# Optimization experiments

Hardware: AMD Instinct MI355X
Metric: run time of the kernel (lower is better)

## Reference

```python
import jax, jax.numpy as jnp
import numpy as np

# IR-Net EDE surrogate-gradient constants (ir_1w1a.IRConv2d defaults)
K = 10.0
T = 0.1
BN_EPS = 1e-5

@jax.custom_vjp
def binary_quantize(x):
    return jnp.sign(x)

def _bq_fwd(x):
    return jnp.sign(x), x

def _bq_bwd(x, g):
    # grad = k * t * (1 - tanh(x*t)^2) * g   (IR-Net BinaryQuantize.backward)
    return (K * T * (1.0 - jnp.tanh(x * T) ** 2) * g,)

binary_quantize.defvjp(_bq_fwd, _bq_bwd)


def setup_inputs() -> dict:
    key = jax.random.key(0)
    k1, k2 = jax.random.split(key, 2)
    return {
        "x": jax.random.normal(k1, (32, 256, 56, 56), dtype=jnp.float32),
        "weight": jax.random.normal(k2, (256, 256, 3, 3), dtype=jnp.float32) * 0.05,
        "gamma": jnp.ones((256,), dtype=jnp.float32),
        "beta": jnp.zeros((256,), dtype=jnp.float32),
    }


def _convalg(x, weight, gamma, beta):
    co = weight.shape[0]
    wf = weight.reshape(co, -1)
    # per-output-channel standardization of weights
    bw = weight - wf.mean(-1).reshape(co, 1, 1, 1)
    std = jnp.std(bw.reshape(co, -1), axis=-1, ddof=1).reshape(co, 1, 1, 1)  # torch unbiased std
    bw = bw / std
    # detached power-of-2 per-channel scale: sw = 2^round(log2(mean|bw|))
    sw = jax.lax.stop_gradient(
        2.0 ** jnp.round(jnp.log2(jnp.abs(bw).reshape(co, -1).mean(-1)))
    ).reshape(co, 1, 1, 1)
    bwq = binary_quantize(bw) * sw   # binarized, scaled weights {-sw, +sw}
    ba = binary_quantize(x)          # binarized activations {-1, +1}
    y = jax.lax.conv_general_dilated(
        ba, bwq,
        window_strides=(1, 1),
        padding=((1, 1), (1, 1)),
        dimension_numbers=("NCHW", "OIHW", "NCHW"),
    )
    # BatchNorm2d, training-mode forward (batch statistics, biased variance)
    mean = y.mean(axis=(0, 2, 3), keepdims=True)
    var = y.var(axis=(0, 2, 3), keepdims=True)
    yn = (y - mean) * jax.lax.rsqrt(var + BN_EPS)
    yn = yn * gamma.reshape(1, -1, 1, 1) + beta.reshape(1, -1, 1, 1)
    # Hardtanh
    return jnp.clip(yn, -1.0, 1.0)


def reference(x, weight, gamma, beta):
    return _convalg(x, weight, gamma, beta)
```

## Files before the change

### kernel.cpp

```cpp
#include <hip/hip_runtime.h>
#include <math.h>

#define HH 56
#define WW 56
#define NB 32
#define CC 256
#define PIX 3136
#define M_TOT 100352
#define PADH 58
#define PADW 58
#define ACTQ_BYTES ((size_t)NB*PADH*PADW*CC)
#define WQ_BYTES ((size_t)9*CC*CC)
#define SBUF_BYTES ((size_t)M_TOT*CC*2)
#define BM 128
#define BN 256

typedef unsigned int u32;
typedef unsigned long long u64;
typedef int v4i __attribute__((ext_vector_type(4)));

typedef const __attribute__((address_space(1))) unsigned int* as1_u32p;
typedef __attribute__((address_space(3))) unsigned int* as3_u32p;
#define GLOAD_LDS16(g, l) \
  __builtin_amdgcn_global_load_lds((as1_u32p)(g), (as3_u32p)(l), 16, 0, 0)

__global__ __launch_bounds__(256) void pack_weights_i8(
    const float* __restrict__ wt, signed char* __restrict__ wq,
    float* __restrict__ swv,
    long long* __restrict__ sumS, long long* __restrict__ sumSS) {
  int co = blockIdx.x;
  int t  = threadIdx.x;
  int lane = t & 63, wid = t >> 6;

  float wv[9];
  const float* wp = wt + ((size_t)co*CC + t)*9;
  double psum = 0.0;
#pragma unroll
  for (int k = 0; k < 9; ++k) { wv[k] = wp[k]; psum += (double)wv[k]; }

  __shared__ double redm[4];
#pragma unroll
  for (int off = 32; off > 0; off >>= 1) psum += __shfl_xor(psum, off);
  if (lane == 0) redm[wid] = psum;
  __syncthreads();
  double mean = (redm[0]+redm[1]+redm[2]+redm[3]) * (1.0/2304.0);

  double pabs = 0.0, psq = 0.0;
#pragma unroll
  for (int k = 0; k < 9; ++k) {
    double d = (double)wv[k] - mean;
    pabs += fabs(d);
    psq  += d*d;
  }
#pragma unroll
  for (int off = 32; off > 0; off >>= 1) {
    pabs += __shfl_xor(pabs, off);
    psq  += __shfl_xor(psq,  off);
  }
  __shared__ double reda[4], redq[4];
  if (lane == 0) { reda[wid] = pabs; redq[wid] = psq; }
  __syncthreads();
  if (t == 0) {
    double sa = reda[0]+reda[1]+reda[2]+reda[3];
    double sq = redq[0]+redq[1]+redq[2]+redq[3];
    double stdv = sqrt(sq / 2303.0);
    double mabs = (sa * (1.0/2304.0)) / stdv;
    swv[co] = (float)exp2(rint(log2(mabs)));
    sumS[co]  = 0;
    sumSS[co] = 0;
  }
#pragma unroll
  for (int k = 0; k < 9; ++k)
    wq[((size_t)k*CC + co)*CC + t] =
        (((double)wv[k] - mean) > 0.0) ? (signed char)1 : (signed char)-1;
}

__global__ __launch_bounds__(256) void pack_acts_i8(
    const float* __restrict__ x, signed char* __restrict__ actq) {
  int n = blockIdx.y, tile = blockIdx.x;
  int lane = threadIdx.x & 63, cw = threadIdx.x >> 6;
  int pp = tile*64 + lane;
  if (pp >= PADH*PADW) return;
  int ph = pp / PADW, pw = pp - ph*PADW;
  signed char* dst = actq + ((size_t)(n*PADH + ph)*PADW + pw)*CC + cw*64;
  if (ph == 0 || ph == PADH-1 || pw == 0 || pw == PADW-1) {
    uint4 z = make_uint4(0u, 0u, 0u, 0u);
#pragma unroll
    for (int q = 0; q < 4; ++q) ((uint4*)dst)[q] = z;
    return;
  }
  int h = ph - 1, w = pw - 1;
  const float* xp = x + ((size_t)(n*CC + cw*64))*PIX + h*WW + w;
  u32 wrd[16];
#pragma unroll
  for (int c16 = 0; c16 < 16; ++c16) {
    u32 v = 0;
#pragma unroll
    for (int b = 0; b < 4; ++b) {
      float f = xp[(size_t)(c16*4 + b)*PIX];
      v |= (f > 0.0f ? 0x01u : 0xFFu) << (8*b);
    }
    wrd[c16] = v;
  }
#pragma unroll
  for (int q = 0; q < 4; ++q)
    ((uint4*)dst)[q] = make_uint4(wrd[4*q], wrd[4*q+1], wrd[4*q+2], wrd[4*q+3]);
}


#define STAGEM(SN, BUF) do {                                              \
    int tn_ = (SN) >> 2, kn_ = (SN) & 3;                                  \
    int aoff_ = ((tn_/3 - 1)*PADW + (tn_%3 - 1))*CC + kn_*64;             \
    int boff_ = tn_*65536 + kn_*64;                                       \
    char* nb_ = (char*)lds + (BUF)*24576;                                 \
    GLOAD_LDS16(pA0 + aoff_, nb_ + ldst);                                 \
    GLOAD_LDS16(pA1 + aoff_, nb_ + 4096 + ldst);                          \
    GLOAD_LDS16(pB0 + boff_, nb_ + 8192 + ldst);                          \
    GLOAD_LDS16(pB1 + boff_, nb_ + 12288 + ldst);                         \
    GLOAD_LDS16(pB2 + boff_, nb_ + 16384 + ldst);                         \
    GLOAD_LDS16(pB3 + boff_, nb_ + 20480 + ldst);                         \
  } while (0)

#define STEPM(S, BUF, WTXT, DOSTAGE) do {                                 \
    asm volatile("s_waitcnt " WTXT ::: "memory");                         \
    __builtin_amdgcn_s_barrier();                                         \
    const char* cb_ = (const char*)lds + (BUF)*24576;                     \
    v4i af[4], bf[8];                                                     \
    _Pragma("unroll")                                                     \
    for (int i = 0; i < 4; ++i)                                           \
      af[i] = *(const v4i*)(cb_ + (ar0 + i*16 + lm)*64 + rdo);            \
    _Pragma("unroll")                                                     \
    for (int j = 0; j < 8; ++j)                                           \
      bf[j] = *(const v4i*)(cb_ + 8192 + (bc0 + j*16 + lm)*64 + rdo);     \
    asm volatile("s_waitcnt lgkmcnt(0)" ::: "memory");                    \
    __builtin_amdgcn_s_barrier();                                         \
    if (DOSTAGE) { STAGEM((S) + 3, BUF); }                                \
    __builtin_amdgcn_s_setprio(1);                                        \
    _Pragma("unroll")                                                     \
    for (int i = 0; i < 4; ++i)                                           \
      _Pragma("unroll")                                                   \
      for (int j = 0; j < 8; ++j)                                         \
        acc[i][j] = __builtin_amdgcn_mfma_i32_16x16x64_i8(af[i], bf[j],   \
                                                          acc[i][j], 0, 0, 0); \
    __builtin_amdgcn_s_setprio(0);                                        \
  } while (0)

template <bool S16>
__global__ __launch_bounds__(256, 2) void bconv_mfma(
    const signed char* __restrict__ actq, const signed char* __restrict__ wq,
    short* __restrict__ s16out, float* __restrict__ f32out,
    u64* __restrict__ sumS, u64* __restrict__ sumSS) {
  __shared__ char lds[73728] __attribute__((aligned(16)));
  __shared__ int colS[256], colQ[256];

  int t = threadIdx.x;
  int lane = t & 63, wv = t >> 6;
  int lm = lane & 15, quad = lane >> 4;
  int ar0 = (wv & 1) * 64;
  int bc0 = (wv >> 1) * 128;
  int Mbase = blockIdx.x * BM;

  colS[t] = 0; colQ[t] = 0;

  int r = t >> 2, c16 = t & 3;
  int cs = c16 ^ ((r >> 1) & 3);
  const signed char *pA0, *pA1;
  {
    int P = Mbase + r;
    int n_ = P / PIX, pl_ = P % PIX, h_ = pl_ / WW, w_ = pl_ % WW;
    pA0 = actq + ((size_t)(n_*PADH + h_+1)*PADW + (w_+1))*CC + cs*16;
    P += 64;
    n_ = P / PIX; pl_ = P % PIX; h_ = pl_ / WW; w_ = pl_ % WW;
    pA1 = actq + ((size_t)(n_*PADH + h_+1)*PADW + (w_+1))*CC + cs*16;
  }
  const signed char* pB0 = wq + (size_t)r*CC + cs*16;
  const signed char* pB1 = pB0 +  64*CC;
  const signed char* pB2 = pB0 + 128*CC;
  const signed char* pB3 = pB0 + 192*CC;
  int ldst = t*16;

  int rdo = (quad ^ ((lm >> 1) & 3)) * 16;

  v4i acc[4][8];
#pragma unroll
  for (int i = 0; i < 4; ++i)
#pragma unroll
    for (int j = 0; j < 8; ++j) acc[i][j] = 0;

  STAGEM(0, 0);
  STAGEM(1, 1);
  STAGEM(2, 2);

#pragma unroll 1
  for (int s = 0; s < 33; s += 3) {
    STEPM(s,     0, "vmcnt(12)", true);
    STEPM(s + 1, 1, "vmcnt(12)", true);
    STEPM(s + 2, 2, "vmcnt(12)", true);
  }
  STEPM(33, 0, "vmcnt(12)", false);
  STEPM(34, 1, "vmcnt(6)",  false);
  STEPM(35, 2, "vmcnt(0)",  false);

  int Sl[8] = {0,0,0,0,0,0,0,0}, Ql[8] = {0,0,0,0,0,0,0,0};
#pragma unroll
  for (int i = 0; i < 4; ++i) {
    int R = Mbase + ar0 + i*16 + quad*4;
    int nR = R / PIX, plR = R % PIX;
#pragma unroll
    for (int j = 0; j < 8; ++j) {
      int colo = bc0 + j*16 + lm;
      v4i a = acc[i][j];
      size_t idx = ((size_t)nR*CC + colo)*PIX + plR;
      if (S16) {
        int2 pk;
        pk.x = (a.x & 0xFFFF) | (a.y << 16);
        pk.y = (a.z & 0xFFFF) | (a.w << 16);
        *(int2*)(s16out + idx) = pk;
      } else {
        *(float4*)(f32out + idx) =
            make_float4((float)a.x, (float)a.y, (float)a.z, (float)a.w);
      }
      Sl[j] += a.x + a.y + a.z + a.w;
      Ql[j] += a.x*a.x + a.y*a.y + a.z*a.z + a.w*a.w;
    }
  }
#pragma unroll
  for (int j = 0; j < 8; ++j) {
    int S = Sl[j], Q = Ql[j];
    S += __shfl_xor(S, 16); S += __shfl_xor(S, 32);
    Q += __shfl_xor(Q, 16); Q += __shfl_xor(Q, 32);
    if (quad == 0) {
      atomicAdd(&colS[bc0 + j*16 + lm], S);
      atomicAdd(&colQ[bc0 + j*16 + lm], Q);
    }
  }
  __syncthreads();
  atomicAdd(&sumS[t], (u64)(long long)colS[t]);
  atomicAdd(&sumSS[t], (u64)(long long)colQ[t]);
}

__global__ void finalize_stats(
    const long long* __restrict__ sumS, const long long* __restrict__ sumSS,
    const float* __restrict__ swv,
    const float* __restrict__ gamma, const float* __restrict__ beta,
    float* __restrict__ AB) {
  int c = threadIdx.x;
  double mu  = (double)sumS[c]  / (double)M_TOT;
  double var = (double)sumSS[c] / (double)M_TOT - mu*mu;
  double sw  = (double)swv[c];
  double inv = 1.0 / sqrt(sw*sw*var + 1e-5);
  double scale = (double)gamma[c] * sw * inv;
  double shift = (double)beta[c] - scale * mu;
  AB[c]      = (float)scale;
  AB[CC + c] = (float)shift;
}

__global__ __launch_bounds__(256) void bn_apply_s16(
    const short* __restrict__ s, float* __restrict__ out,
    const float* __restrict__ AB, int n8) {
  int i = blockIdx.x*256 + threadIdx.x;
  if (i >= n8) return;
  union { int4 v; short sh[8]; } u;
  u.v = ((const int4*)s)[i];
  int c = ((i*8) / PIX) & (CC-1);
  float a = AB[c], b = AB[CC + c];
  float4 o0, o1;
  o0.x = fminf(1.f, fmaxf(-1.f, (float)u.sh[0]*a + b));
  o0.y = fminf(1.f, fmaxf(-1.f, (float)u.sh[1]*a + b));
  o0.z = fminf(1.f, fmaxf(-1.f, (float)u.sh[2]*a + b));
  o0.w = fminf(1.f, fmaxf(-1.f, (float)u.sh[3]*a + b));
  o1.x = fminf(1.f, fmaxf(-1.f, (float)u.sh[4]*a + b));
  o1.y = fminf(1.f, fmaxf(-1.f, (float)u.sh[5]*a + b));
  o1.z = fminf(1.f, fmaxf(-1.f, (float)u.sh[6]*a + b));
  o1.w = fminf(1.f, fmaxf(-1.f, (float)u.sh[7]*a + b));
  ((float4*)out)[2*i]   = o0;
  ((float4*)out)[2*i+1] = o1;
}

__global__ __launch_bounds__(256) void bn_apply_f32(
    float* __restrict__ out, const float* __restrict__ AB, int n4) {
  int i = blockIdx.x*256 + threadIdx.x;
  if (i >= n4) return;
  float4 v = ((float4*)out)[i];
  int c = ((i*4) / PIX) & (CC-1);
  float a = AB[c], b = AB[CC + c];
  v.x = fminf(1.f, fmaxf(-1.f, v.x*a + b));
  v.y = fminf(1.f, fmaxf(-1.f, v.y*a + b));
  v.z = fminf(1.f, fmaxf(-1.f, v.z*a + b));
  v.w = fminf(1.f, fmaxf(-1.f, v.w*a + b));
  ((float4*)out)[i] = v;
}

extern "C" void kernel_launch(void* const* d_in, const int* in_sizes, int n_in,
                              void* d_out, int out_size, void* d_ws, size_t ws_size,
                              hipStream_t stream) {
  (void)in_sizes; (void)n_in; (void)out_size;
  const float* x     = (const float*)d_in[0];
  const float* wt    = (const float*)d_in[1];
  const float* gamma = (const float*)d_in[2];
  const float* beta  = (const float*)d_in[3];
  float* out = (float*)d_out;

  char* ws = (char*)d_ws;
  size_t off = 0;
  signed char* actq = (signed char*)(ws + off);
  off += ACTQ_BYTES;             off = (off + 255) & ~(size_t)255;
  signed char* wq = (signed char*)(ws + off);
  off += WQ_BYTES;               off = (off + 255) & ~(size_t)255;
  float* swv = (float*)(ws + off); off += 1024;
  float* AB  = (float*)(ws + off); off += 2048;
  long long* sumS  = (long long*)(ws + off); off += 2048;
  long long* sumSS = (long long*)(ws + off); off += 2048;
  off = (off + 255) & ~(size_t)255;
  short* sbuf = (short*)(ws + off);
  bool s16 = (ws_size >= off + SBUF_BYTES);

  pack_weights_i8<<<256, 256, 0, stream>>>(wt, wq, swv, sumS, sumSS);
  pack_acts_i8<<<dim3(53, NB), 256, 0, stream>>>(x, actq);
  if (s16) {
    bconv_mfma<true><<<dim3(M_TOT/BM, 1), 256, 0, stream>>>(
        actq, wq, sbuf, nullptr, (u64*)sumS, (u64*)sumSS);
  } else {
    bconv_mfma<false><<<dim3(M_TOT/BM, 1), 256, 0, stream>>>(
        actq, wq, nullptr, out, (u64*)sumS, (u64*)sumSS);
  }
  finalize_stats<<<1, 256, 0, stream>>>(sumS, sumSS, swv, gamma, beta, AB);
  if (s16) {
    bn_apply_s16<<<(M_TOT*CC/8 + 255)/256, 256, 0, stream>>>(
        sbuf, out, AB, M_TOT*CC/8);
  } else {
    bn_apply_f32<<<(M_TOT*CC/4 + 255)/256, 256, 0, stream>>>(
        out, AB, M_TOT*CC/4);
  }
}
```

Measured before the change: 153.0 us.

## Load activation MFMA fragments directly from global into registers, bypassing LDS

Each wave's A-operand (activation) fragments are now read straight from global memory into registers, double-buffered one k-step ahead. Only the weight tile is still staged through LDS with async global-to-LDS loads, which shrinks the LDS footprint and removes the A-side LDS reads. The aim is to cut LDS traffic and capacity so the loads overlap better with compute. In exchange, the two column-half waves each load the same activation rows from global memory, the vmcnt waits become tighter, and more registers are used for the prefetched fragments.

```diff
diff --git a/kernel.cpp b/kernel.cpp
--- a/kernel.cpp
+++ b/kernel.cpp
@@ -108,39 +108,44 @@
 }
 
 
-#define STAGEM(SN, BUF) do {                                              \
+#define STAGEMB(SN, BUF) do {                                             \
+    int tn_ = (SN) >> 2, kn_ = (SN) & 3;                                  \
+    int boff_ = tn_*65536 + kn_*64;                                       \
+    char* nb_ = (char*)lds + (BUF)*16384;                                 \
+    GLOAD_LDS16(pB0 + boff_, nb_ + ldst);                                 \
+    GLOAD_LDS16(pB1 + boff_, nb_ + 4096 + ldst);                         \
+    GLOAD_LDS16(pB2 + boff_, nb_ + 8192 + ldst);                          \
+    GLOAD_LDS16(pB3 + boff_, nb_ + 12288 + ldst);                        \
+  } while (0)
+
+#define ASTAGE(SN, AF) do {                                               \
     int tn_ = (SN) >> 2, kn_ = (SN) & 3;                                  \
     int aoff_ = ((tn_/3 - 1)*PADW + (tn_%3 - 1))*CC + kn_*64;             \
-    int boff_ = tn_*65536 + kn_*64;                                       \
-    char* nb_ = (char*)lds + (BUF)*24576;                                 \
-    GLOAD_LDS16(pA0 + aoff_, nb_ + ldst);                                 \
-    GLOAD_LDS16(pA1 + aoff_, nb_ + 4096 + ldst);                          \
-    GLOAD_LDS16(pB0 + boff_, nb_ + 8192 + ldst);                          \
-    GLOAD_LDS16(pB1 + boff_, nb_ + 12288 + ldst);                         \
-    GLOAD_LDS16(pB2 + boff_, nb_ + 16384 + ldst);                         \
-    GLOAD_LDS16(pB3 + boff_, nb_ + 20480 + ldst);                         \
+    AF[0] = *(const v4i*)(pA0g + aoff_);                                  \
+    AF[1] = *(const v4i*)(pA1g + aoff_);                                  \
+    AF[2] = *(const v4i*)(pA2g + aoff_);                                  \
+    AF[3] = *(const v4i*)(pA3g + aoff_);                                  \
   } while (0)
 
-#define STEPM(S, BUF, WTXT, DOSTAGE) do {                                 \
+#define STEP(S, BUF, AFC, AFN, WTXT, DOB, DOA) do {                       \
     asm volatile("s_waitcnt " WTXT ::: "memory");                         \
     __builtin_amdgcn_s_barrier();                                         \
-    const char* cb_ = (const char*)lds + (BUF)*24576;                     \
-    v4i af[4], bf[8];                                                     \
-    _Pragma("unroll")                                                     \
-    for (int i = 0; i < 4; ++i)                                           \
-      af[i] = *(const v4i*)(cb_ + (ar0 + i*16 + lm)*64 + rdo);            \
+    if (DOA) { ASTAGE((S) + 1, AFN); }                                    \
+    __builtin_amdgcn_sched_barrier(0);                                    \
+    const char* cb_ = (const char*)lds + (BUF)*16384;                     \
+    v4i bf[8];                                                            \
     _Pragma("unroll")                                                     \
     for (int j = 0; j < 8; ++j)                                           \
-      bf[j] = *(const v4i*)(cb_ + 8192 + (bc0 + j*16 + lm)*64 + rdo);     \
+      bf[j] = *(const v4i*)(cb_ + (bc0 + j*16 + lm)*64 + rdo);            \
     asm volatile("s_waitcnt lgkmcnt(0)" ::: "memory");                    \
     __builtin_amdgcn_s_barrier();                                         \
-    if (DOSTAGE) { STAGEM((S) + 3, BUF); }                                \
+    if (DOB) { STAGEMB((S) + 3, BUF); }                                   \
     __builtin_amdgcn_s_setprio(1);                                        \
     _Pragma("unroll")                                                     \
     for (int i = 0; i < 4; ++i)                                           \
       _Pragma("unroll")                                                   \
       for (int j = 0; j < 8; ++j)                                         \
-        acc[i][j] = __builtin_amdgcn_mfma_i32_16x16x64_i8(af[i], bf[j],   \
+        acc[i][j] = __builtin_amdgcn_mfma_i32_16x16x64_i8(AFC[i], bf[j],  \
                                                           acc[i][j], 0, 0, 0); \
     __builtin_amdgcn_s_setprio(0);                                        \
   } while (0)
@@ -150,7 +155,7 @@
     const signed char* __restrict__ actq, const signed char* __restrict__ wq,
     short* __restrict__ s16out, float* __restrict__ f32out,
     u64* __restrict__ sumS, u64* __restrict__ sumSS) {
-  __shared__ char lds[73728] __attribute__((aligned(16)));
+  __shared__ char lds[49152] __attribute__((aligned(16)));
   __shared__ int colS[256], colQ[256];
 
   int t = threadIdx.x;
@@ -164,15 +169,6 @@
 
   int r = t >> 2, c16 = t & 3;
   int cs = c16 ^ ((r >> 1) & 3);
-  const signed char *pA0, *pA1;
-  {
-    int P = Mbase + r;
-    int n_ = P / PIX, pl_ = P % PIX, h_ = pl_ / WW, w_ = pl_ % WW;
-    pA0 = actq + ((size_t)(n_*PADH + h_+1)*PADW + (w_+1))*CC + cs*16;
-    P += 64;
-    n_ = P / PIX; pl_ = P % PIX; h_ = pl_ / WW; w_ = pl_ % WW;
-    pA1 = actq + ((size_t)(n_*PADH + h_+1)*PADW + (w_+1))*CC + cs*16;
-  }
   const signed char* pB0 = wq + (size_t)r*CC + cs*16;
   const signed char* pB1 = pB0 +  64*CC;
   const signed char* pB2 = pB0 + 128*CC;
@@ -181,25 +177,54 @@
 
   int rdo = (quad ^ ((lm >> 1) & 3)) * 16;
 
+  const signed char *pA0g, *pA1g, *pA2g, *pA3g;
+  {
+    int P0 = Mbase + ar0 + lm;
+#define MKPA(PVAR, DST) {                                                  \
+      int n_ = (PVAR) / PIX, pl_ = (PVAR) % PIX;                           \
+      int h_ = pl_ / WW, w_ = pl_ - h_*WW;                                 \
+      DST = actq + ((size_t)(n_*PADH + h_+1)*PADW + (w_+1))*CC + quad*16; }
+    MKPA(P0,      pA0g);
+    MKPA(P0 + 16, pA1g);
+    MKPA(P0 + 32, pA2g);
+    MKPA(P0 + 48, pA3g);
+#undef MKPA
+  }
+
   v4i acc[4][8];
 #pragma unroll
   for (int i = 0; i < 4; ++i)
 #pragma unroll
     for (int j = 0; j < 8; ++j) acc[i][j] = 0;
 
-  STAGEM(0, 0);
-  STAGEM(1, 1);
-  STAGEM(2, 2);
-
+  v4i af0[4], af1[4];
+
+  STAGEMB(0, 0);
+  STAGEMB(1, 1);
+  STAGEMB(2, 2);
+  ASTAGE(0, af0);
+
+  STEP(0, 0, af0, af1, "vmcnt(0)", 1, 1);
+  STEP(1, 1, af1, af0, "vmcnt(4)", 1, 1);
+  STEP(2, 2, af0, af1, "vmcnt(4)", 1, 1);
+  STEP(3, 0, af1, af0, "vmcnt(4)", 1, 1);
+  STEP(4, 1, af0, af1, "vmcnt(4)", 1, 1);
+  STEP(5, 2, af1, af0, "vmcnt(4)", 1, 1);
 #pragma unroll 1
-  for (int s = 0; s < 33; s += 3) {
-    STEPM(s,     0, "vmcnt(12)", true);
-    STEPM(s + 1, 1, "vmcnt(12)", true);
-    STEPM(s + 2, 2, "vmcnt(12)", true);
-  }
-  STEPM(33, 0, "vmcnt(12)", false);
-  STEPM(34, 1, "vmcnt(6)",  false);
-  STEPM(35, 2, "vmcnt(0)",  false);
+  for (int s = 6; s < 30; s += 6) {
+    STEP(s + 0, 0, af0, af1, "vmcnt(4)", 1, 1);
+    STEP(s + 1, 1, af1, af0, "vmcnt(4)", 1, 1);
+    STEP(s + 2, 2, af0, af1, "vmcnt(4)", 1, 1);
+    STEP(s + 3, 0, af1, af0, "vmcnt(4)", 1, 1);
+    STEP(s + 4, 1, af0, af1, "vmcnt(4)", 1, 1);
+    STEP(s + 5, 2, af1, af0, "vmcnt(4)", 1, 1);
+  }
+  STEP(30, 0, af0, af1, "vmcnt(4)", 1, 1);
+  STEP(31, 1, af1, af0, "vmcnt(4)", 1, 1);
+  STEP(32, 2, af0, af1, "vmcnt(4)", 1, 1);
+  STEP(33, 0, af1, af0, "vmcnt(4)", 0, 1);
+  STEP(34, 1, af0, af1, "vmcnt(0)", 0, 1);
+  STEP(35, 2, af1, af0, "vmcnt(0)", 0, 0);
 
   int Sl[8] = {0,0,0,0,0,0,0,0}, Ql[8] = {0,0,0,0,0,0,0,0};
 #pragma unroll
```

Measured after the change: 212.2 us. +38.7%, slower.
